# Optimization experiments

Hardware: AMD Instinct MI355X
Metric: run time of the kernel (lower is better)

The kernel has to match this reference:

```python
import jax, jax.numpy as jnp
import numpy as np
from jax import lax

L, B, S, D, H = 2, 8, 2048, 1024, 1024
LOG_H0 = float(np.log(0.5))  # h0 = g(0) = 0.5


def _log_g(x):
    # log of g(x) = x + 0.5 if x >= 0 else sigmoid(x)
    return jnp.where(x >= 0, jnp.log(jnp.where(x >= 0, x + 0.5, 1.0)), -jax.nn.softplus(-x))


def _mingru_layer(x, Wz, bz, Wh, bh):
    # x: (B,S,D) -> (B,S,H) via log-space heinsen associative scan
    k = jnp.einsum('bsd,hd->bsh', x, Wz) + bz          # gate pre-activation
    log_z = -jax.nn.softplus(-k)                        # log sigmoid(k)
    log_coeffs = -jax.nn.softplus(k)                    # log (1 - sigmoid(k))
    pre_h = jnp.einsum('bsd,hd->bsh', x, Wh) + bh
    log_values = log_z + _log_g(pre_h)                  # log(z * h_tilde)
    Bq = x.shape[0]
    # prepend initial state: coeff 0 (log 1), value log(h0)
    log_coeffs = jnp.pad(log_coeffs, ((0, 0), (1, 0), (0, 0)))
    log_values = jnp.concatenate(
        [jnp.full((Bq, 1, log_values.shape[-1]), LOG_H0, dtype=log_values.dtype), log_values], axis=1)
    a_star = jnp.cumsum(log_coeffs, axis=1)
    log_h = a_star + lax.cumlogsumexp(log_values - a_star, axis=1)
    return jnp.exp(log_h)[:, 1:]


def setup_inputs() -> dict:
    key = jax.random.key(0)
    ks = jax.random.split(key, 5)
    stdv = 1.0 / np.sqrt(D)
    u = lambda k, shp: jax.random.uniform(k, shp, jnp.float32, -stdv, stdv)
    return {
        'x': jax.random.normal(ks[0], (B, S, D), jnp.float32),
        'Wz': u(ks[1], (L, H, D)),
        'bz': u(ks[2], (L, H)),
        'Wh': u(ks[3], (L, H, D)),
        'bh': u(ks[4], (L, H)),
    }


def reference(x, Wz, bz, Wh, bh):
    h = x
    for l in range(Wz.shape[0]):
        h = _mingru_layer(h, Wz[l], bz[l], Wh[l], bh[l])
    return h  # (B,S,H), last layer outputs
```

## Files before the change

kernel.cpp:

```cpp
#include <hip/hip_runtime.h>
#include <hip/hip_bf16.h>


#define L_ 2
#define B_ 8
#define S_ 2048
#define D_ 1024
#define H_ 1024
#define M_ (B_*S_)
#define NC 32
#define CL (S_/NC)

typedef __bf16    bf16x8 __attribute__((ext_vector_type(8)));
typedef float     f32x4  __attribute__((ext_vector_type(4)));
typedef _Float16  h2     __attribute__((ext_vector_type(2)));
typedef _Float16  h8     __attribute__((ext_vector_type(8)));

__device__ __forceinline__ ushort f2bf(float f) {
    union { __hip_bfloat16 h; ushort u; } c;
    c.h = __float2bfloat16(f);
    return c.u;
}

__device__ __forceinline__ void async16(const void* g, void* l) {
    __builtin_amdgcn_global_load_lds(
        (const __attribute__((address_space(1))) unsigned int*)g,
        (__attribute__((address_space(3))) unsigned int*)l, 16, 0, 0);
}

__global__ __launch_bounds__(256) void cast_all(const float* __restrict__ x,
                                                const float* __restrict__ Wz,
                                                const float* __restrict__ Wh,
                                                ushort* __restrict__ xb,
                                                ushort* __restrict__ wzb,
                                                ushort* __restrict__ whb) {
    const int nw = L_*H_*D_/4;
    int i = blockIdx.x * 256 + threadIdx.x;
    {
        float4 v = ((const float4*)x)[i];
        ushort4 o;
        o.x = f2bf(v.x); o.y = f2bf(v.y); o.z = f2bf(v.z); o.w = f2bf(v.w);
        ((ushort4*)xb)[i] = o;
    }
    if (i < nw) {
        float4 v = ((const float4*)Wz)[i];
        ushort4 o;
        o.x = f2bf(v.x); o.y = f2bf(v.y); o.z = f2bf(v.z); o.w = f2bf(v.w);
        ((ushort4*)wzb)[i] = o;
        float4 w = ((const float4*)Wh)[i];
        ushort4 p;
        p.x = f2bf(w.x); p.y = f2bf(w.y); p.z = f2bf(w.z); p.w = f2bf(w.w);
        ((ushort4*)whb)[i] = p;
    }
}

#define SWZ(R, c) (((R) << 6) + ((((c) ^ ((R) & 7))) << 3))
#define MFMA16 __builtin_amdgcn_mfma_f32_16x16x32_bf16
#define FENCE() asm volatile("" ::: "memory")

__global__ __launch_bounds__(256) void gemm_fused(const ushort* __restrict__ A,
                                                  const ushort* __restrict__ Wz,
                                                  const ushort* __restrict__ Wh,
                                                  const float* __restrict__ bz,
                                                  const float* __restrict__ bh,
                                                  h2* __restrict__ cv,
                                                  float* __restrict__ Ac,
                                                  float* __restrict__ Bc)
{
    extern __shared__ __align__(16) ushort sm[];

    const int t    = threadIdx.x;
    const int lane = t & 63;
    const int wave = t >> 6;
    const int xcd = (int)blockIdx.x & 7;
    const int k8  = (int)blockIdx.x >> 3;
    const int nblk = k8 & 15;
    const int mblk = ((k8 >> 4) << 3) + xcd;
    const int m0 = mblk * 128;
    const int n0 = nblk * 64;
    const int wm = (wave >> 1) * 64;
    const int wn = (wave & 1) * 32;

    const int srow   = lane >> 3;
    const int scol_g = (((lane & 7) ^ srow) << 3);

    f32x4 accz[4][2] = {};
    f32x4 acch[4][2] = {};
    const int lrow = lane & 15;
    const int lcq  = lane >> 4;

    #define STAGE(kb, bo)                                                      \
        do {                                                                   \
            _Pragma("unroll")                                                  \
            for (int i_ = 0; i_ < 4; ++i_) {                  \
                int r_ = i_*32 + wave*8;                                       \
                async16(&A[(size_t)(m0 + r_ + srow)*D_ + (kb) + scol_g],       \
                        &sm[(bo) + r_*64]);                                    \
            }                                                                  \
            _Pragma("unroll")                                                  \
            for (int i_ = 0; i_ < 2; ++i_) {              \
                int r_ = i_*32 + wave*8;                                       \
                async16(&Wz[(size_t)(n0 + r_ + srow)*D_ + (kb) + scol_g],      \
                        &sm[(bo) + 8192 + r_*64]);                             \
                async16(&Wh[(size_t)(n0 + r_ + srow)*D_ + (kb) + scol_g],      \
                        &sm[(bo) + 12288 + r_*64]);                            \
            }                                                                  \
        } while (0)

    STAGE(0, 0);

    #pragma unroll 2
    for (int tt = 0; tt < 16; ++tt) {
        const int cur = (tt & 1) << 14;
        const int nxt = cur ^ 16384;
        const int kbn = (tt < 15 ? tt + 1 : 15) << 6;
        STAGE(kbn, nxt);
        asm volatile("s_waitcnt vmcnt(8)" ::: "memory");
        __builtin_amdgcn_s_barrier();
        FENCE();
        #pragma unroll
        for (int kk = 0; kk < 64; kk += 32) {
            const int cq = (kk >> 3) + lcq;
            bf16x8 af[4];
            #pragma unroll
            for (int mt = 0; mt < 4; ++mt) {
                int R = wm + mt*16 + lrow;
                uint4 u = *(const uint4*)&sm[cur + SWZ(R, cq)];
                af[mt] = __builtin_bit_cast(bf16x8, u);
            }
            #pragma unroll
            for (int nt = 0; nt < 2; ++nt) {
                int R = wn + nt*16 + lrow;
                uint4 uz = *(const uint4*)&sm[cur + 8192  + SWZ(R, cq)];
                uint4 uh = *(const uint4*)&sm[cur + 12288 + SWZ(R, cq)];
                bf16x8 zb = __builtin_bit_cast(bf16x8, uz);
                bf16x8 hb = __builtin_bit_cast(bf16x8, uh);
                #pragma unroll
                for (int mt = 0; mt < 4; ++mt) {
                    accz[mt][nt] = MFMA16(af[mt], zb, accz[mt][nt], 0, 0, 0);
                    acch[mt][nt] = MFMA16(af[mt], hb, acch[mt][nt], 0, 0, 0);
                }
            }
        }
        FENCE();
        __builtin_amdgcn_s_barrier();
    }

    asm volatile("s_waitcnt vmcnt(0)" ::: "memory");
    __syncthreads();

    float2* seg = (float2*)sm;
    const int colq = lane & 15;
    const int rowq = (lane >> 4) << 2;
    #pragma unroll
    for (int nt = 0; nt < 2; ++nt) {
        const int n = n0 + wn + nt*16 + colq;
        const float bzv = bz[n];
        const float bhv = bh[n];
        #pragma unroll
        for (int mt = 0; mt < 4; ++mt) {
            float a = 1.f, bb = 0.f;
            h8 pk;
            #pragma unroll
            for (int r = 0; r < 4; ++r) {
                float kx = accz[mt][nt][r] + bzv;
                float p  = acch[mt][nt][r] + bhv;
                float e   = __expf(-fabsf(kx));
                float inv = 1.0f / (1.0f + e);
                float z   = (kx >= 0.f) ? inv     : e * inv;
                float c   = (kx >= 0.f) ? e * inv : inv;
                float g;
                if (p >= 0.f) g = p + 0.5f;
                else { float eg = __expf(p); g = eg / (1.0f + eg); }
                float v = z * g;
                pk[2*r]     = (_Float16)c;
                pk[2*r + 1] = (_Float16)v;
                bb = fmaf(c, bb, v);
                a *= c;
            }
            const int mb4 = (m0 + wm + mt*16 + rowq) >> 2;
            *(h8*)&cv[((size_t)mb4 * H_ + n) * 4] = pk;
            const int sidx = (wm >> 2) + mt*4 + (rowq >> 2);
            seg[sidx*65 + wn + nt*16 + colq] = make_float2(a, bb);
        }
    }
    __syncthreads();
    if (t < 128) {
        const int col  = t & 63;
        const int half = t >> 6;
        float a = 1.f, bb = 0.f;
        #pragma unroll
        for (int s = 0; s < 16; ++s) {
            float2 e2 = seg[(half*16 + s)*65 + col];
            bb = fmaf(e2.x, bb, e2.y);
            a *= e2.x;
        }
        const int b     = m0 >> 11;
        const int chunk = ((m0 >> 6) & (NC - 1)) + half;
        const int q = (b*NC + chunk)*H_ + n0 + col;
        Ac[q] = a; Bc[q] = bb;
    }
    #undef STAGE
}

__global__ __launch_bounds__(256) void scan_emit(const h2* __restrict__ cv,
                                                 const float* __restrict__ Ac,
                                                 const float* __restrict__ Bc,
                                                 float* __restrict__ outf,
                                                 ushort* __restrict__ outb,
                                                 const int write_bf16)
{
    int q = blockIdx.x * 256 + threadIdx.x;
    int h = q & (H_-1);
    int c = (q >> 10) & (NC-1);
    int b = q >> 15;
    float hc = 0.5f;
    for (int cp = 0; cp < c; ++cp) {
        int idx = (b*NC + cp)*H_ + h;
        hc = fmaf(Ac[idx], hc, Bc[idx]);
    }
    const int mb = b*S_ + c*CL;
    if (write_bf16) {
        #pragma unroll 4
        for (int j = 0; j < 16; ++j) {
            h8 e = *(const h8*)&cv[(((size_t)(mb >> 2) + j)*H_ + h) * 4];
            #pragma unroll
            for (int u = 0; u < 4; ++u) {
                hc = fmaf((float)e[2*u], hc, (float)e[2*u + 1]);
                outb[(size_t)(mb + 4*j + u)*H_ + h] = f2bf(hc);
            }
        }
    } else {
        #pragma unroll 4
        for (int j = 0; j < 16; ++j) {
            h8 e = *(const h8*)&cv[(((size_t)(mb >> 2) + j)*H_ + h) * 4];
            #pragma unroll
            for (int u = 0; u < 4; ++u) {
                hc = fmaf((float)e[2*u], hc, (float)e[2*u + 1]);
                outf[(size_t)(mb + 4*j + u)*H_ + h] = hc;
            }
        }
    }
}

extern "C" void kernel_launch(void* const* d_in, const int* in_sizes, int n_in,
                              void* d_out, int out_size, void* d_ws, size_t ws_size,
                              hipStream_t stream)
{
    const float* x  = (const float*)d_in[0];
    const float* Wz = (const float*)d_in[1];
    const float* bz = (const float*)d_in[2];
    const float* Wh = (const float*)d_in[3];
    const float* bh = (const float*)d_in[4];
    float* out = (float*)d_out;

    static bool attr_set = false;
    if (!attr_set) {
        (void)hipFuncSetAttribute(reinterpret_cast<const void*>(gemm_fused),
                                  hipFuncAttributeMaxDynamicSharedMemorySize, 65536);
        attr_set = true;
    }

    ushort* xb  = (ushort*)d_ws;
    ushort* wzb = xb  + (size_t)M_*D_;
    ushort* whb = wzb + (size_t)L_*H_*D_;
    h2*     cv  = (h2*)(whb + (size_t)L_*H_*D_);
    float*  Ac  = (float*)(cv + (size_t)M_*H_);
    float*  Bc  = Ac + B_*NC*H_;

    cast_all<<<(M_*D_/4)/256, 256, 0, stream>>>(x, Wz, Wh, xb, wzb, whb);

    const int gemm_grid = (M_/128) * (H_/64);
    for (int l = 0; l < L_; ++l) {
        gemm_fused<<<gemm_grid, 256, 65536, stream>>>(xb,
                                                      wzb + (size_t)l*H_*D_,
                                                      whb + (size_t)l*H_*D_,
                                                      bz + l*H_, bh + l*H_,
                                                      cv, Ac, Bc);
        scan_emit<<<(B_*NC*H_)/256, 256, 0, stream>>>(cv, Ac, Bc, out, xb,
                                                      (l == 0) ? 1 : 0);
    }
}
```

Baseline: 343.6 us.

## Fuse GEMM and scan into a cooperative persistent kernel with grid sync

Replaces the per-layer GEMM plus scan_emit pair with one cooperative kernel of 512 persistent blocks. Each block computes four 128-row tiles, keeps the packed (coeff, value) fp16 pairs in registers, publishes chunk summaries, grid-syncs, then scans and writes outputs directly. This removes the global round trip of the cv intermediate and one kernel launch per layer. In exchange, the LDS double-buffered prefetch pipeline becomes a single buffer, the emit phase runs serially on only 128 threads per block, and register pressure is high. The old two-kernel path is kept as a fallback when occupancy is insufficient.

```diff
diff --git a/kernel.cpp b/kernel.cpp
--- a/kernel.cpp
+++ b/kernel.cpp
@@ -1,5 +1,6 @@
 #include <hip/hip_runtime.h>
 #include <hip/hip_bf16.h>
+#include <hip/hip_cooperative_groups.h>
 
 
 #define L_ 2
@@ -56,18 +57,213 @@
 
 #define SWZ(R, c) (((R) << 6) + ((((c) ^ ((R) & 7))) << 3))
 #define MFMA16 __builtin_amdgcn_mfma_f32_16x16x32_bf16
-#define FENCE() asm volatile("" ::: "memory")
-
-__global__ __launch_bounds__(256) void gemm_fused(const ushort* __restrict__ A,
-                                                  const ushort* __restrict__ Wz,
-                                                  const ushort* __restrict__ Wh,
-                                                  const float* __restrict__ bz,
-                                                  const float* __restrict__ bh,
-                                                  h2* __restrict__ cv,
-                                                  float* __restrict__ Ac,
-                                                  float* __restrict__ Bc)
+
+__global__ __launch_bounds__(256, 2) void mingru_layer(const ushort* A,
+                                                       const ushort* __restrict__ Wz,
+                                                       const ushort* __restrict__ Wh,
+                                                       const float* __restrict__ bz,
+                                                       const float* __restrict__ bh,
+                                                       float* Ac,
+                                                       float* Bc,
+                                                       float* outf,
+                                                       ushort* outb,
+                                                       int write_bf16)
 {
     extern __shared__ __align__(16) ushort sm[];
+
+    const int t    = threadIdx.x;
+    const int lane = t & 63;
+    const int wave = t >> 6;
+    const int bid  = (int)blockIdx.x;
+    const int xcd  = bid & 7;
+    const int q8   = bid >> 3;
+    const int nblk = q8 & 15;
+    const int pg   = q8 >> 4;
+    const int panel = pg*8 + xcd;
+    const int b    = panel >> 2;
+    const int mg   = panel & 3;
+    const int n0 = nblk * 64;
+    const int wm = (wave >> 1) * 64;
+    const int wn = (wave & 1) * 32;
+
+    const int srow   = lane >> 3;
+    const int scol_g = (((lane & 7) ^ srow) << 3);
+    const int lrow = lane & 15;
+    const int lcq  = lane >> 4;
+    const int colq = lane & 15;
+    const int rowq = (lane >> 4) << 2;
+
+    float bzv[2], bhv[2];
+    #pragma unroll
+    for (int nt = 0; nt < 2; ++nt) {
+        const int n = n0 + wn + nt*16 + colq;
+        bzv[nt] = bz[n];
+        bhv[nt] = bh[n];
+    }
+
+    h8 cvr[4][8];
+
+    #pragma unroll
+    for (int ti = 0; ti < 4; ++ti) {
+        const int tloc = mg*4 + ti;
+        const int m0 = b*S_ + tloc*128;
+
+        f32x4 accz[4][2] = {};
+        f32x4 acch[4][2] = {};
+
+        for (int kb = 0; kb < D_; kb += 64) {
+            __syncthreads();
+            #pragma unroll
+            for (int i_ = 0; i_ < 4; ++i_) {
+                int r_ = i_*32 + wave*8;
+                async16(&A[(size_t)(m0 + r_ + srow)*D_ + kb + scol_g], &sm[r_*64]);
+            }
+            #pragma unroll
+            for (int i_ = 0; i_ < 2; ++i_) {
+                int r_ = i_*32 + wave*8;
+                async16(&Wz[(size_t)(n0 + r_ + srow)*D_ + kb + scol_g], &sm[8192  + r_*64]);
+                async16(&Wh[(size_t)(n0 + r_ + srow)*D_ + kb + scol_g], &sm[12288 + r_*64]);
+            }
+            __syncthreads();
+            #pragma unroll
+            for (int kk = 0; kk < 64; kk += 32) {
+                const int cq = (kk >> 3) + lcq;
+                bf16x8 af[4];
+                #pragma unroll
+                for (int mt = 0; mt < 4; ++mt) {
+                    int R = wm + mt*16 + lrow;
+                    uint4 u = *(const uint4*)&sm[SWZ(R, cq)];
+                    af[mt] = __builtin_bit_cast(bf16x8, u);
+                }
+                #pragma unroll
+                for (int nt = 0; nt < 2; ++nt) {
+                    int R = wn + nt*16 + lrow;
+                    uint4 uz = *(const uint4*)&sm[8192  + SWZ(R, cq)];
+                    uint4 uh = *(const uint4*)&sm[12288 + SWZ(R, cq)];
+                    bf16x8 zb = __builtin_bit_cast(bf16x8, uz);
+                    bf16x8 hb = __builtin_bit_cast(bf16x8, uh);
+                    #pragma unroll
+                    for (int mt = 0; mt < 4; ++mt) {
+                        accz[mt][nt] = MFMA16(af[mt], zb, accz[mt][nt], 0, 0, 0);
+                        acch[mt][nt] = MFMA16(af[mt], hb, acch[mt][nt], 0, 0, 0);
+                    }
+                }
+            }
+        }
+
+        __syncthreads();
+        float2* seg = (float2*)sm;
+        #pragma unroll
+        for (int nt = 0; nt < 2; ++nt) {
+            #pragma unroll
+            for (int mt = 0; mt < 4; ++mt) {
+                float a = 1.f, bb = 0.f;
+                h8 pk;
+                #pragma unroll
+                for (int r = 0; r < 4; ++r) {
+                    float kx = accz[mt][nt][r] + bzv[nt];
+                    float p  = acch[mt][nt][r] + bhv[nt];
+                    float e   = __expf(-fabsf(kx));
+                    float inv = 1.0f / (1.0f + e);
+                    float z   = (kx >= 0.f) ? inv     : e * inv;
+                    float c   = (kx >= 0.f) ? e * inv : inv;
+                    float g;
+                    if (p >= 0.f) g = p + 0.5f;
+                    else { float eg = __expf(p); g = eg / (1.0f + eg); }
+                    float v = z * g;
+                    pk[2*r]     = (_Float16)c;
+                    pk[2*r + 1] = (_Float16)v;
+                    bb = fmaf(c, bb, v);
+                    a *= c;
+                }
+                cvr[ti][nt*4 + mt] = pk;
+                const int sidx = (wm >> 2) + mt*4 + (rowq >> 2);
+                seg[sidx*65 + wn + nt*16 + colq] = make_float2(a, bb);
+            }
+        }
+        __syncthreads();
+        if (t < 128) {
+            const int col  = t & 63;
+            const int half = t >> 6;
+            float a = 1.f, bb = 0.f;
+            #pragma unroll
+            for (int s = 0; s < 16; ++s) {
+                float2 e2 = seg[(half*16 + s)*65 + col];
+                bb = fmaf(e2.x, bb, e2.y);
+                a *= e2.x;
+            }
+            const int chunk = tloc*2 + half;
+            const int qi = (b*NC + chunk)*H_ + n0 + col;
+            __hip_atomic_store(&Ac[qi], a,  __ATOMIC_RELAXED, __HIP_MEMORY_SCOPE_AGENT);
+            __hip_atomic_store(&Bc[qi], bb, __ATOMIC_RELAXED, __HIP_MEMORY_SCOPE_AGENT);
+        }
+    }
+
+    __threadfence();
+    cooperative_groups::this_grid().sync();
+
+    h2* cvlds = (h2*)sm;
+    #pragma unroll
+    for (int ti = 0; ti < 4; ++ti) {
+        const int tloc = mg*4 + ti;
+        const int m0 = b*S_ + tloc*128;
+        __syncthreads();
+        #pragma unroll
+        for (int nt = 0; nt < 2; ++nt) {
+            const int coll = wn + nt*16 + colq;
+            #pragma unroll
+            for (int mt = 0; mt < 4; ++mt) {
+                h8 pk = cvr[ti][nt*4 + mt];
+                #pragma unroll
+                for (int r = 0; r < 4; ++r) {
+                    const int rr = wm + mt*16 + rowq + r;
+                    h2 e; e[0] = pk[2*r]; e[1] = pk[2*r + 1];
+                    cvlds[rr*64 + coll] = e;
+                }
+            }
+        }
+        __syncthreads();
+        if (t < 128) {
+            const int col = t & 63;
+            const int ck  = t >> 6;
+            const int cg  = tloc*2 + ck;
+            float hc = 0.5f;
+            for (int cp = 0; cp < cg; ++cp) {
+                int idx = (b*NC + cp)*H_ + n0 + col;
+                float av = __hip_atomic_load(&Ac[idx], __ATOMIC_RELAXED, __HIP_MEMORY_SCOPE_AGENT);
+                float bv = __hip_atomic_load(&Bc[idx], __ATOMIC_RELAXED, __HIP_MEMORY_SCOPE_AGENT);
+                hc = fmaf(av, hc, bv);
+            }
+            const size_t gbase = (size_t)(m0 + ck*64)*H_ + n0 + col;
+            if (write_bf16) {
+                #pragma unroll 4
+                for (int row = 0; row < 64; ++row) {
+                    h2 e = cvlds[(ck*64 + row)*64 + col];
+                    hc = fmaf((float)e[0], hc, (float)e[1]);
+                    outb[gbase + (size_t)row*H_] = f2bf(hc);
+                }
+            } else {
+                #pragma unroll 4
+                for (int row = 0; row < 64; ++row) {
+                    h2 e = cvlds[(ck*64 + row)*64 + col];
+                    hc = fmaf((float)e[0], hc, (float)e[1]);
+                    outf[gbase + (size_t)row*H_] = hc;
+                }
+            }
+        }
+    }
+}
+
+__global__ __launch_bounds__(256) void gemm_fb(const ushort* __restrict__ A,
+                                               const ushort* __restrict__ Wz,
+                                               const ushort* __restrict__ Wh,
+                                               const float* __restrict__ bz,
+                                               const float* __restrict__ bh,
+                                               h2* __restrict__ cv,
+                                               float* __restrict__ Ac,
+                                               float* __restrict__ Bc)
+{
+    __shared__ __align__(16) ushort sm[16384];
 
     const int t    = threadIdx.x;
     const int lane = t & 63;
@@ -89,35 +285,20 @@
     const int lrow = lane & 15;
     const int lcq  = lane >> 4;
 
-    #define STAGE(kb, bo)                                                      \
-        do {                                                                   \
-            _Pragma("unroll")                                                  \
-            for (int i_ = 0; i_ < 4; ++i_) {                  \
-                int r_ = i_*32 + wave*8;                                       \
-                async16(&A[(size_t)(m0 + r_ + srow)*D_ + (kb) + scol_g],       \
-                        &sm[(bo) + r_*64]);                                    \
-            }                                                                  \
-            _Pragma("unroll")                                                  \
-            for (int i_ = 0; i_ < 2; ++i_) {              \
-                int r_ = i_*32 + wave*8;                                       \
-                async16(&Wz[(size_t)(n0 + r_ + srow)*D_ + (kb) + scol_g],      \
-                        &sm[(bo) + 8192 + r_*64]);                             \
-                async16(&Wh[(size_t)(n0 + r_ + srow)*D_ + (kb) + scol_g],      \
-                        &sm[(bo) + 12288 + r_*64]);                            \
-            }                                                                  \
-        } while (0)
-
-    STAGE(0, 0);
-
-    #pragma unroll 2
-    for (int tt = 0; tt < 16; ++tt) {
-        const int cur = (tt & 1) << 14;
-        const int nxt = cur ^ 16384;
-        const int kbn = (tt < 15 ? tt + 1 : 15) << 6;
-        STAGE(kbn, nxt);
-        asm volatile("s_waitcnt vmcnt(8)" ::: "memory");
-        __builtin_amdgcn_s_barrier();
-        FENCE();
+    for (int kb = 0; kb < D_; kb += 64) {
+        __syncthreads();
+        #pragma unroll
+        for (int i = 0; i < 4; ++i) {
+            int r = i*32 + wave*8;
+            async16(&A[(size_t)(m0 + r + srow)*D_ + kb + scol_g], &sm[r*64]);
+        }
+        #pragma unroll
+        for (int i = 0; i < 2; ++i) {
+            int r = i*32 + wave*8;
+            async16(&Wz[(size_t)(n0 + r + srow)*D_ + kb + scol_g], &sm[8192  + r*64]);
+            async16(&Wh[(size_t)(n0 + r + srow)*D_ + kb + scol_g], &sm[12288 + r*64]);
+        }
+        __syncthreads();
         #pragma unroll
         for (int kk = 0; kk < 64; kk += 32) {
             const int cq = (kk >> 3) + lcq;
@@ -125,14 +306,14 @@
             #pragma unroll
             for (int mt = 0; mt < 4; ++mt) {
                 int R = wm + mt*16 + lrow;
-                uint4 u = *(const uint4*)&sm[cur + SWZ(R, cq)];
+                uint4 u = *(const uint4*)&sm[SWZ(R, cq)];
                 af[mt] = __builtin_bit_cast(bf16x8, u);
             }
             #pragma unroll
             for (int nt = 0; nt < 2; ++nt) {
                 int R = wn + nt*16 + lrow;
-                uint4 uz = *(const uint4*)&sm[cur + 8192  + SWZ(R, cq)];
-                uint4 uh = *(const uint4*)&sm[cur + 12288 + SWZ(R, cq)];
+                uint4 uz = *(const uint4*)&sm[8192  + SWZ(R, cq)];
+                uint4 uh = *(const uint4*)&sm[12288 + SWZ(R, cq)];
                 bf16x8 zb = __builtin_bit_cast(bf16x8, uz);
                 bf16x8 hb = __builtin_bit_cast(bf16x8, uh);
                 #pragma unroll
@@ -142,13 +323,9 @@
                 }
             }
         }
-        FENCE();
-        __builtin_amdgcn_s_barrier();
-    }
-
-    asm volatile("s_waitcnt vmcnt(0)" ::: "memory");
+    }
+
     __syncthreads();
-
     float2* seg = (float2*)sm;
     const int colq = lane & 15;
     const int rowq = (lane >> 4) << 2;
@@ -200,15 +377,14 @@
         const int q = (b*NC + chunk)*H_ + n0 + col;
         Ac[q] = a; Bc[q] = bb;
     }
-    #undef STAGE
-}
-
-__global__ __launch_bounds__(256) void scan_emit(const h2* __restrict__ cv,
-                                                 const float* __restrict__ Ac,
-                                                 const float* __restrict__ Bc,
-                                                 float* __restrict__ outf,
-                                                 ushort* __restrict__ outb,
-                                                 const int write_bf16)
+}
+
+__global__ __launch_bounds__(256) void scan_emit_fb(const h2* __restrict__ cv,
+                                                    const float* __restrict__ Ac,
+                                                    const float* __restrict__ Bc,
+                                                    float* __restrict__ outf,
+                                                    ushort* __restrict__ outb,
+                                                    const int write_bf16)
 {
     int q = blockIdx.x * 256 + threadIdx.x;
     int h = q & (H_-1);
@@ -254,13 +430,6 @@
     const float* bh = (const float*)d_in[4];
     float* out = (float*)d_out;
 
-    static bool attr_set = false;
-    if (!attr_set) {
-        (void)hipFuncSetAttribute(reinterpret_cast<const void*>(gemm_fused),
-                                  hipFuncAttributeMaxDynamicSharedMemorySize, 65536);
-        attr_set = true;
-    }
-
     ushort* xb  = (ushort*)d_ws;
     ushort* wzb = xb  + (size_t)M_*D_;
     ushort* whb = wzb + (size_t)L_*H_*D_;
@@ -268,16 +437,42 @@
     float*  Ac  = (float*)(cv + (size_t)M_*H_);
     float*  Bc  = Ac + B_*NC*H_;
 
+    static int coop_ok = -1;
+    if (coop_ok < 0) {
+        int nb = 0;
+        hipError_t e = hipOccupancyMaxActiveBlocksPerMultiprocessor(
+            &nb, reinterpret_cast<const void*>(mingru_layer), 256, (size_t)32768);
+        coop_ok = (e == hipSuccess && nb >= 2) ? 1 : 0;
+    }
+
     cast_all<<<(M_*D_/4)/256, 256, 0, stream>>>(x, Wz, Wh, xb, wzb, whb);
 
-    const int gemm_grid = (M_/128) * (H_/64);
-    for (int l = 0; l < L_; ++l) {
-        gemm_fused<<<gemm_grid, 256, 65536, stream>>>(xb,
-                                                      wzb + (size_t)l*H_*D_,
-                                                      whb + (size_t)l*H_*D_,
-                                                      bz + l*H_, bh + l*H_,
-                                                      cv, Ac, Bc);
-        scan_emit<<<(B_*NC*H_)/256, 256, 0, stream>>>(cv, Ac, Bc, out, xb,
-                                                      (l == 0) ? 1 : 0);
-    }
-}
+    if (coop_ok) {
+        for (int l = 0; l < L_; ++l) {
+            const ushort* A_  = xb;
+            const ushort* Wz_ = wzb + (size_t)l*H_*D_;
+            const ushort* Wh_ = whb + (size_t)l*H_*D_;
+            const float*  bz_ = bz + l*H_;
+            const float*  bh_ = bh + l*H_;
+            float*  Ac_ = Ac;
+            float*  Bc_ = Bc;
+            float*  of_ = out;
+            ushort* ob_ = xb;
+            int wb = (l == 0) ? 1 : 0;
+            void* args[] = {&A_, &Wz_, &Wh_, &bz_, &bh_, &Ac_, &Bc_, &of_, &ob_, &wb};
+            hipLaunchCooperativeKernel(reinterpret_cast<const void*>(mingru_layer),
+                                       dim3(512), dim3(256), args, 32768, stream);
+        }
+    } else {
+        const int gemm_grid = (M_/128) * (H_/64);
+        for (int l = 0; l < L_; ++l) {
+            gemm_fb<<<gemm_grid, 256, 0, stream>>>(xb,
+                                                   wzb + (size_t)l*H_*D_,
+                                                   whb + (size_t)l*H_*D_,
+                                                   bz + l*H_, bh + l*H_,
+                                                   cv, Ac, Bc);
+            scan_emit_fb<<<(B_*NC*H_)/256, 256, 0, stream>>>(cv, Ac, Bc, out, xb,
+                                                             (l == 0) ? 1 : 0);
+        }
+    }
+}
```

Result: no change. 337.5 us (-1.8%).
